# Kernel tuning notes

Hardware: AMD Instinct MI355X
Metric: run time of the kernel (lower is better)

Reference implementation:

```python
import jax, jax.numpy as jnp
import numpy as np

FEATURE_DIM, HIDDEN_DIM, ATTN_DIM = 2048, 1024, 1024
B, L = 128, 196


def setup_inputs() -> dict:
    key = jax.random.key(0)
    ks = jax.random.split(key, 8)
    s_enc = 1.0 / np.sqrt(FEATURE_DIM)
    s_hid = 1.0 / np.sqrt(HIDDEN_DIM)
    s_full = 1.0 / np.sqrt(ATTN_DIM)
    return {
        "encoder_out": jax.random.normal(ks[0], (B, L, FEATURE_DIM), jnp.float32),
        "hidden": jax.random.normal(ks[1], (B, HIDDEN_DIM), jnp.float32),
        "W_enc": jax.random.uniform(ks[2], (FEATURE_DIM, ATTN_DIM), jnp.float32, -s_enc, s_enc),
        "b_enc": jax.random.uniform(ks[3], (ATTN_DIM,), jnp.float32, -s_enc, s_enc),
        "W_hid": jax.random.uniform(ks[4], (HIDDEN_DIM, ATTN_DIM), jnp.float32, -s_hid, s_hid),
        "b_hid": jax.random.uniform(ks[5], (ATTN_DIM,), jnp.float32, -s_hid, s_hid),
        "W_full": jax.random.uniform(ks[6], (ATTN_DIM,), jnp.float32, -s_full, s_full),
        "b_full": jax.random.uniform(ks[7], (1,), jnp.float32, -s_full, s_full),
    }


def reference(encoder_out, hidden, W_enc, b_enc, W_hid, b_hid, W_full, b_full):
    # attn1: (B, L, A)
    attn1 = jnp.einsum("blf,fa->bla", encoder_out, W_enc) + b_enc
    # attn2: (B, 1, A)
    attn2 = (hidden @ W_hid + b_hid)[:, None, :]
    attn = jax.nn.relu(attn1 + attn2)
    # scalar score per location: (B, L)
    scores = jnp.einsum("bla,a->bl", attn, W_full) + b_full[0]
    alpha = jax.nn.softmax(scores, axis=1)
    # weighted sum over L: (B, F)
    context = jnp.einsum("blf,bl->bf", encoder_out, alpha)
    return context, alpha
```

## Files before the change

kernel.cpp:

```cpp
#include <hip/hip_runtime.h>
#include <hip/hip_bf16.h>

typedef unsigned short u16;
typedef short s16x8 __attribute__((ext_vector_type(8)));
typedef unsigned int u32x2 __attribute__((ext_vector_type(2)));
typedef unsigned int u32x4 __attribute__((ext_vector_type(4)));
typedef float f32x4 __attribute__((ext_vector_type(4)));

#define F_DIM 2048
#define A_DIM 1024
#define H_DIM 1024
#define BATCH 128
#define LLEN  196
#define MROWS (BATCH * LLEN)
#define MTILES (MROWS / 256)

__device__ __forceinline__ u16 f2b(float x) {
  union { float f; unsigned int u; } c; c.f = x;
  unsigned int r = (c.u + 0x7fffu + ((c.u >> 16) & 1u)) >> 16;
  return (u16)r;
}

__device__ __forceinline__ unsigned int f2b_pk(float a, float b) {
  unsigned int r;
  asm volatile("v_cvt_pk_bf16_f32 %0, %1, %2" : "=v"(r) : "v"(a), "v"(b));
  return r;
}

__device__ __forceinline__ void gload_lds16(const void* g, void* l) {
  __builtin_amdgcn_global_load_lds((const __attribute__((address_space(1))) void*)g,
                                   (__attribute__((address_space(3))) void*)l, 16, 0, 0);
}

__global__ __launch_bounds__(256) void prep_kernel(
    const float* __restrict__ W, u16* __restrict__ WT,
    const float* __restrict__ hidden, const float* __restrict__ W_hid,
    const float* __restrict__ b_hid, const float* __restrict__ b_enc,
    float* __restrict__ attn2p,
    const float* __restrict__ enc, u16* __restrict__ encB) {
  int t = threadIdx.x;
  if (blockIdx.x < 2048) {
    __shared__ float tile[32][33];
    int id = blockIdx.x;
    int kb = (id & 63) * 32, ab = (id >> 6) * 32;
    int r = t >> 3, c = (t & 7) * 4;
    float4 v = *(const float4*)&W[(size_t)(kb + r) * A_DIM + ab + c];
    tile[r][c] = v.x; tile[r][c + 1] = v.y; tile[r][c + 2] = v.z; tile[r][c + 3] = v.w;
    __syncthreads();
    ushort4 o;
    o.x = f2b(tile[c + 0][r]);
    o.y = f2b(tile[c + 1][r]);
    o.z = f2b(tile[c + 2][r]);
    o.w = f2b(tile[c + 3][r]);
    *(ushort4*)&WT[(size_t)(ab + r) * F_DIM + kb + c] = o;
  } else if (blockIdx.x < 2560) {
    __shared__ float hl[8][128];
    int id = blockIdx.x - 2048;
    int a  = (id & 3) * 256 + t;
    int b0 = ((id >> 2) & 15) * 8;
    int k0 = (id >> 6) * 128;
    {
      int j = t >> 5, kk = (t & 31) * 4;
      float4 v = *(const float4*)&hidden[(size_t)(b0 + j) * H_DIM + k0 + kk];
      hl[j][kk + 0] = v.x; hl[j][kk + 1] = v.y; hl[j][kk + 2] = v.z; hl[j][kk + 3] = v.w;
    }
    __syncthreads();
    float acc[8] = {0.f, 0.f, 0.f, 0.f, 0.f, 0.f, 0.f, 0.f};
    #pragma unroll 4
    for (int k = 0; k < 128; ++k) {
      float w = W_hid[(size_t)(k0 + k) * A_DIM + a];
      #pragma unroll
      for (int j = 0; j < 8; ++j) acc[j] = fmaf(hl[j][k], w, acc[j]);
    }
    if ((id >> 6) == 0) {
      float bias = b_hid[a] + b_enc[a];
      #pragma unroll
      for (int j = 0; j < 8; ++j) acc[j] += bias;
    }
    #pragma unroll
    for (int j = 0; j < 8; ++j) atomicAdd(&attn2p[(size_t)(b0 + j) * A_DIM + a], acc[j]);
  } else {
    const size_t n8 = (size_t)MROWS * F_DIM / 8;
    size_t gid = (size_t)(blockIdx.x - 2560) * 256 + t;
    for (size_t k = gid; k < n8; k += (size_t)2048 * 256) {
      const float4* sp = (const float4*)enc + k * 2;
      float4 a = sp[0], b = sp[1];
      u32x4 w;
      w.x = f2b_pk(a.x, a.y); w.y = f2b_pk(a.z, a.w);
      w.z = f2b_pk(b.x, b.y); w.w = f2b_pk(b.z, b.w);
      *(u32x4*)(encB + k * 8) = w;
    }
  }
}

__global__ __launch_bounds__(512, 2) void gemm_score_a(
    const u16* __restrict__ encB, const u16* __restrict__ WT,
    const float* __restrict__ attn2p, const float* __restrict__ W_full,
    float* __restrict__ scores) {
  __shared__ __align__(16) u16 As[4 * 8192];
  __shared__ __align__(16) u16 Bs[4 * 8192];

  int i = blockIdx.x;
  int g = i >> 5, r = i & 31;
  int y = r >> 3, gi = r & 7;
  int mt = g * 8 + gi;
  if (mt >= MTILES) return;
  int m0 = mt * 256, n0 = y * 256;
  int t = threadIdx.x;
  int lane = t & 63, wave = t >> 6;
  int wr = wave >> 2, wc = wave & 3;
  int c16 = lane & 15, quad = lane >> 4;

  const u16* agp = encB + (size_t)(m0 + (t >> 2)) * F_DIM + ((t & 3) ^ ((t >> 3) & 3)) * 8;
  const u16* bgp = WT   + (size_t)(n0 + (t >> 2)) * F_DIM + ((t & 3) ^ ((t >> 3) & 3)) * 8;

  const int gsw = (quad ^ ((c16 >> 1) & 3)) * 8;
  const int aro = (wr * 128 + c16) * 32;
  const int bro = (wc * 64 + c16) * 32;

  f32x4 acc[8][4];
  #pragma unroll
  for (int mi = 0; mi < 8; ++mi)
    #pragma unroll
    for (int ni = 0; ni < 4; ++ni) acc[mi][ni] = (f32x4){0.f, 0.f, 0.f, 0.f};

  s16x8 af[4], bf[4];

#define AGL(cb, kt_) do {                                                       \
    _Pragma("unroll")                                                           \
    for (int s_ = 0; s_ < 2; ++s_)                                              \
      gload_lds16(agp + (size_t)s_ * 128 * F_DIM + (size_t)(kt_) * 32,          \
                  As + (cb) * 8192 + s_ * 4096 + wave * 512);                   \
  } while (0)

#define BGL(cb, kt_) do {                                                       \
    _Pragma("unroll")                                                           \
    for (int s_ = 0; s_ < 2; ++s_)                                              \
      gload_lds16(bgp + (size_t)s_ * 128 * F_DIM + (size_t)(kt_) * 32,          \
                  Bs + (cb) * 8192 + s_ * 4096 + wave * 512);                   \
  } while (0)

#define DSRA(cb, mh)                                                            \
    _Pragma("unroll")                                                           \
    for (int i_ = 0; i_ < 4; ++i_)                                              \
      af[i_] = *(const s16x8*)&As[(cb) * 8192 + aro + ((mh) * 4 + i_) * 512 + gsw];

#define DSRB(cb)                                                                \
    _Pragma("unroll")                                                           \
    for (int j_ = 0; j_ < 4; ++j_)                                              \
      bf[j_] = *(const s16x8*)&Bs[(cb) * 8192 + bro + j_ * 512 + gsw];

#define PHTAIL(mh) do {                                                         \
    __builtin_amdgcn_s_barrier();                                               \
    asm volatile("s_waitcnt lgkmcnt(0)" ::: "memory");                          \
    __builtin_amdgcn_s_setprio(1);                                              \
    _Pragma("unroll")                                                           \
    for (int i_ = 0; i_ < 4; ++i_)                                              \
      _Pragma("unroll")                                                         \
      for (int j_ = 0; j_ < 4; ++j_)                                            \
        acc[(mh) * 4 + i_][j_] =                                                \
            __builtin_amdgcn_mfma_f32_16x16x32_bf16(                            \
                af[i_], bf[j_], acc[(mh) * 4 + i_][j_], 0, 0, 0);               \
    __builtin_amdgcn_s_setprio(0);                                              \
    __builtin_amdgcn_s_barrier();                                               \
  } while (0)

#define TILE(T_, RB_, WB_) do {                                                 \
    int kS_ = min((T_) + 2, 63);                                                \
     DSRA(RB_, 0); DSRB(RB_); AGL(WB_, kS_); PHTAIL(0);                 \
     DSRA(RB_, 1); BGL(WB_, kS_);                                       \
    asm volatile("s_waitcnt vmcnt(4)" ::: "memory");                            \
    PHTAIL(1);                                                                  \
  } while (0)

  AGL(0, 0); BGL(0, 0);
  AGL(1, 1); BGL(1, 1);
  asm volatile("s_waitcnt vmcnt(4)" ::: "memory");
  __builtin_amdgcn_s_barrier();

  #pragma unroll 1
  for (int T = 0; T < 64; T += 4) {
    TILE(T,     0, 2);
    TILE(T + 1, 1, 3);
    TILE(T + 2, 2, 0);
    TILE(T + 3, 3, 1);
  }
#undef TILE
#undef PHTAIL
#undef DSRA
#undef DSRB
#undef BGL
#undef AGL

  int bfirst = m0 / LLEN;
  int bnd1 = (bfirst + 1) * LLEN, bnd2 = (bfirst + 2) * LLEN;
  int b1c = min(bfirst + 1, BATCH - 1), b2c = min(bfirst + 2, BATCH - 1);
  float wf[4], a2v0[4], a2v1[4], a2v2[4];
  #pragma unroll
  for (int ni = 0; ni < 4; ++ni) {
    int col = n0 + wc * 64 + ni * 16 + c16;
    wf[ni]   = W_full[col];
    a2v0[ni] = attn2p[(size_t)bfirst * A_DIM + col];
    a2v1[ni] = attn2p[(size_t)b1c * A_DIM + col];
    a2v2[ni] = attn2p[(size_t)b2c * A_DIM + col];
  }
  #pragma unroll
  for (int mi = 0; mi < 8; ++mi) {
    #pragma unroll
    for (int rr = 0; rr < 4; ++rr) {
      int row_g = m0 + wr * 128 + mi * 16 + quad * 4 + rr;
      float p = 0.f;
      #pragma unroll
      for (int ni = 0; ni < 4; ++ni) {
        float a2 = row_g >= bnd1 ? (row_g >= bnd2 ? a2v2[ni] : a2v1[ni]) : a2v0[ni];
        float v = acc[mi][ni][rr] + a2;
        v = fmaxf(v, 0.f);
        p = fmaf(v, wf[ni], p);
      }
      p += __shfl_xor(p, 1);
      p += __shfl_xor(p, 2);
      p += __shfl_xor(p, 4);
      p += __shfl_xor(p, 8);
      if (c16 == 0) atomicAdd(&scores[row_g], p);
    }
  }
}

__global__ __launch_bounds__(512, 2) void gemm_score_b(
    const float* __restrict__ enc, const u16* __restrict__ WT,
    const float* __restrict__ attn2p, const float* __restrict__ W_full,
    float* __restrict__ scores) {
  __shared__ __align__(16) u16 As[2 * 16384];
  __shared__ __align__(16) u16 Bs[2 * 16384];

  int i = blockIdx.x;
  int g = i >> 5, r = i & 31;
  int y = r >> 3, gi = r & 7;
  int mt = g * 8 + gi;
  if (mt >= MTILES) return;
  int m0 = mt * 256, n0 = y * 256;
  int t = threadIdx.x;
  int lane = t & 63, wave = t >> 6;
  int wr = wave >> 2, wc = wave & 3;
  int c16 = lane & 15, quad = lane >> 4;

  const float* aP = enc + (size_t)(m0 + (t >> 2)) * F_DIM + (t & 3) * 4;
  int awo[4];
  #pragma unroll
  for (int s = 0; s < 4; ++s)
    awo[s] = (t >> 2) * 64 + ((t & 3) & 1) * 4
           + (((s * 2 + ((t & 3) >> 1)) ^ ((t >> 2) & 7)) * 8);
  const u16* bgp = WT + (size_t)(n0 + (t >> 3)) * F_DIM + ((t & 7) ^ ((t >> 3) & 7)) * 8;

  const int akey = c16 & 7;
  int gsw[2];
  gsw[0] = ((0 * 4 + quad) ^ akey) * 8;
  gsw[1] = ((1 * 4 + quad) ^ akey) * 8;
  const int aro = (wr * 128 + c16) * 64;
  const int bro = (wc * 64 + c16) * 64;

  f32x4 acc[8][4];
  #pragma unroll
  for (int mi = 0; mi < 8; ++mi)
    #pragma unroll
    for (int ni = 0; ni < 4; ++ni) acc[mi][ni] = (f32x4){0.f, 0.f, 0.f, 0.f};

  s16x8 af[4][2], bf[2][2];
  float4 R0lo[4], R0hi[4], R1lo[4], R1hi[4];

#define ALD(RX, half, kt_) do {                                                 \
    const float* p_ = aP + (size_t)(half) * 128 * F_DIM + (kt_) * 64;           \
    RX[0] = *(const float4*)(p_);                                               \
    RX[1] = *(const float4*)(p_ + 16);                                          \
    RX[2] = *(const float4*)(p_ + 32);                                          \
    RX[3] = *(const float4*)(p_ + 48);                                          \
  } while (0)

#define AWR(RX, cb, half) do {                                                  \
    _Pragma("unroll")                                                           \
    for (int s_ = 0; s_ < 4; ++s_) {                                            \
      u32x2 w_; w_.x = f2b_pk(RX[s_].x, RX[s_].y);                              \
      w_.y = f2b_pk(RX[s_].z, RX[s_].w);                                        \
      *(u32x2*)&As[(cb) * 16384 + (half) * 8192 + awo[s_]] = w_;                \
    }                                                                           \
  } while (0)

#define BGL(cb, kt_) do {                                                       \
    _Pragma("unroll")                                                           \
    for (int s_ = 0; s_ < 4; ++s_)                                              \
      gload_lds16(bgp + (size_t)s_ * 64 * F_DIM + (size_t)(kt_) * 64,           \
                  Bs + (cb) * 16384 + s_ * 4096 + wave * 512);                  \
  } while (0)

#define DSRA(cb, mh)                                                            \
    _Pragma("unroll")                                                           \
    for (int i_ = 0; i_ < 4; ++i_)                                              \
      _Pragma("unroll")                                                         \
      for (int h_ = 0; h_ < 2; ++h_)                                            \
        af[i_][h_] = *(const s16x8*)&As[(cb) * 16384 + aro                      \
                                        + ((mh) * 4 + i_) * 1024 + gsw[h_]];

#define DSRB(cb, nh)                                                            \
    _Pragma("unroll")                                                           \
    for (int j_ = 0; j_ < 2; ++j_)                                              \
      _Pragma("unroll")                                                         \
      for (int h_ = 0; h_ < 2; ++h_)                                            \
        bf[j_][h_] = *(const s16x8*)&Bs[(cb) * 16384 + bro                      \
                                        + ((nh) * 2 + j_) * 1024 + gsw[h_]];

#define PHTAIL(mh, nh) do {                                                     \
    __builtin_amdgcn_s_barrier();                                               \
    asm volatile("s_waitcnt lgkmcnt(0)" ::: "memory");                          \
    __builtin_amdgcn_s_setprio(1);                                              \
    _Pragma("unroll")                                                           \
    for (int i_ = 0; i_ < 4; ++i_)                                              \
      _Pragma("unroll")                                                         \
      for (int j_ = 0; j_ < 2; ++j_)                                            \
        _Pragma("unroll")                                                       \
        for (int h_ = 0; h_ < 2; ++h_)                                          \
          acc[(mh) * 4 + i_][(nh) * 2 + j_] =                                   \
              __builtin_amdgcn_mfma_f32_16x16x32_bf16(                          \
                  af[i_][h_], bf[j_][h_],                                       \
                  acc[(mh) * 4 + i_][(nh) * 2 + j_], 0, 0, 0);                  \
    __builtin_amdgcn_s_setprio(0);                                              \
    __builtin_amdgcn_s_barrier();                                               \
  } while (0)

#define GROUP(T_, RB_, WB_, WLO_, WHI_, LLO_, LHI_) do {                        \
    int kB_ = min((T_) + 1, 31);                                                \
    int kA_ = min((T_) + 2, 31);                                                \
     DSRA(RB_, 0); DSRB(RB_, 0); AWR(WLO_, WB_, 0); BGL(WB_, kB_);      \
    PHTAIL(0, 0);                                                               \
     DSRB(RB_, 1); AWR(WHI_, WB_, 1); ALD(LLO_, 0, kA_);                \
    PHTAIL(0, 1);                                                               \
     DSRA(RB_, 1); DSRB(RB_, 0); ALD(LHI_, 1, kA_);                     \
    PHTAIL(1, 0);                                                               \
     DSRB(RB_, 1);                                                      \
    asm volatile("s_waitcnt vmcnt(8)" ::: "memory");                            \
    PHTAIL(1, 1);                                                               \
  } while (0)

  ALD(R0lo, 0, 0);
  ALD(R0hi, 1, 0);
  BGL(0, 0);
  asm volatile("s_waitcnt vmcnt(4)" ::: "memory");
  AWR(R0lo, 0, 0);
  AWR(R0hi, 0, 1);
  ALD(R1lo, 0, 1);
  ALD(R1hi, 1, 1);
  asm volatile("s_waitcnt vmcnt(8) lgkmcnt(0)" ::: "memory");
  __builtin_amdgcn_s_barrier();

  #pragma unroll 1
  for (int T = 0; T < 32; T += 2) {
    GROUP(T,     0, 1, R1lo, R1hi, R0lo, R0hi);
    GROUP(T + 1, 1, 0, R0lo, R0hi, R1lo, R1hi);
  }
#undef GROUP
#undef PHTAIL
#undef DSRA
#undef DSRB
#undef BGL
#undef AWR
#undef ALD

  int bfirst = m0 / LLEN;
  int bnd1 = (bfirst + 1) * LLEN, bnd2 = (bfirst + 2) * LLEN;
  int b1c = min(bfirst + 1, BATCH - 1), b2c = min(bfirst + 2, BATCH - 1);
  float wf[4], a2v0[4], a2v1[4], a2v2[4];
  #pragma unroll
  for (int ni = 0; ni < 4; ++ni) {
    int col = n0 + wc * 64 + ni * 16 + c16;
    wf[ni]   = W_full[col];
    a2v0[ni] = attn2p[(size_t)bfirst * A_DIM + col];
    a2v1[ni] = attn2p[(size_t)b1c * A_DIM + col];
    a2v2[ni] = attn2p[(size_t)b2c * A_DIM + col];
  }
  #pragma unroll
  for (int mi = 0; mi < 8; ++mi) {
    #pragma unroll
    for (int rr = 0; rr < 4; ++rr) {
      int row_g = m0 + wr * 128 + mi * 16 + quad * 4 + rr;
      float p = 0.f;
      #pragma unroll
      for (int ni = 0; ni < 4; ++ni) {
        float a2 = row_g >= bnd1 ? (row_g >= bnd2 ? a2v2[ni] : a2v1[ni]) : a2v0[ni];
        float v = acc[mi][ni][rr] + a2;
        v = fmaxf(v, 0.f);
        p = fmaf(v, wf[ni], p);
      }
      p += __shfl_xor(p, 1);
      p += __shfl_xor(p, 2);
      p += __shfl_xor(p, 4);
      p += __shfl_xor(p, 8);
      if (c16 == 0) atomicAdd(&scores[row_g], p);
    }
  }
}

__global__ __launch_bounds__(256) void context_kernel(
    const float* __restrict__ enc, const float* __restrict__ scores,
    float* __restrict__ alpha_out, float* __restrict__ out) {
  __shared__ float al[LLEN];
  __shared__ float red[8];
  __shared__ float4 part[4][64];
  int b = blockIdx.y, t = threadIdx.x;
  float s = (t < LLEN) ? scores[b * LLEN + t] : -3.0e38f;
  float m = s;
  #pragma unroll
  for (int o = 1; o <= 32; o <<= 1) m = fmaxf(m, __shfl_xor(m, o));
  if ((t & 63) == 0) red[t >> 6] = m;
  __syncthreads();
  m = fmaxf(fmaxf(red[0], red[1]), fmaxf(red[2], red[3]));
  float e = (t < LLEN) ? expf(s - m) : 0.f;
  float sum = e;
  #pragma unroll
  for (int o = 1; o <= 32; o <<= 1) sum += __shfl_xor(sum, o);
  if ((t & 63) == 0) red[4 + (t >> 6)] = sum;
  __syncthreads();
  sum = red[4] + red[5] + red[6] + red[7];
  float av = e / sum;
  if (t < LLEN) {
    al[t] = av;
    if (blockIdx.x == 0) alpha_out[b * LLEN + t] = av;
  }
  __syncthreads();
  int f4 = blockIdx.x * 64 + (t & 63);
  int lq = t >> 6;
  const float4* e4 = (const float4*)enc
                   + ((size_t)b * LLEN + lq * 49) * (F_DIM / 4) + f4;
  float4 acc = {0.f, 0.f, 0.f, 0.f};
  #pragma unroll 7
  for (int j = 0; j < 49; ++j) {
    float4 v = e4[(size_t)j * (F_DIM / 4)];
    float a = al[lq * 49 + j];
    acc.x = fmaf(v.x, a, acc.x);
    acc.y = fmaf(v.y, a, acc.y);
    acc.z = fmaf(v.z, a, acc.z);
    acc.w = fmaf(v.w, a, acc.w);
  }
  part[lq][t & 63] = acc;
  __syncthreads();
  if (t < 64) {
    float4 p0 = part[0][t], p1 = part[1][t], p2 = part[2][t], p3 = part[3][t];
    float4 sv;
    sv.x = (p0.x + p1.x) + (p2.x + p3.x);
    sv.y = (p0.y + p1.y) + (p2.y + p3.y);
    sv.z = (p0.z + p1.z) + (p2.z + p3.z);
    sv.w = (p0.w + p1.w) + (p2.w + p3.w);
    *(float4*)(out + (size_t)b * F_DIM + (size_t)(blockIdx.x * 64 + t) * 4) = sv;
  }
}

extern "C" void kernel_launch(void* const* d_in, const int* in_sizes, int n_in,
                              void* d_out, int out_size, void* d_ws, size_t ws_size,
                              hipStream_t stream) {
  const float* enc    = (const float*)d_in[0];
  const float* hidden = (const float*)d_in[1];
  const float* W_enc  = (const float*)d_in[2];
  const float* b_enc  = (const float*)d_in[3];
  const float* W_hid  = (const float*)d_in[4];
  const float* b_hid  = (const float*)d_in[5];
  const float* W_full = (const float*)d_in[6];
  float* out = (float*)d_out;
  float* alpha_out = out + (size_t)BATCH * F_DIM;

  const size_t wt_bytes   = (size_t)A_DIM * F_DIM * sizeof(u16);
  const size_t a2_bytes   = (size_t)BATCH * A_DIM * sizeof(float);
  const size_t sc_bytes   = (size_t)MROWS * sizeof(float);
  const size_t encb_bytes = (size_t)MROWS * F_DIM * sizeof(u16);
  char* ws = (char*)d_ws;
  u16*   WT     = (u16*)ws;
  float* attn2p = (float*)(ws + wt_bytes);
  float* scores = (float*)(ws + wt_bytes + a2_bytes);
  u16*   encB   = (u16*)(ws + wt_bytes + a2_bytes + sc_bytes);

  const bool bigws = ws_size >= wt_bytes + a2_bytes + sc_bytes + encb_bytes;

  hipMemsetAsync(attn2p, 0, a2_bytes + sc_bytes, stream);

  if (bigws) {
    prep_kernel<<<dim3(2048 + 512 + 2048), 256, 0, stream>>>(
        W_enc, WT, hidden, W_hid, b_hid, b_enc, attn2p, enc, encB);
    gemm_score_a<<<dim3(416), 512, 0, stream>>>(encB, WT, attn2p, W_full, scores);
  } else {
    prep_kernel<<<dim3(2048 + 512), 256, 0, stream>>>(
        W_enc, WT, hidden, W_hid, b_hid, b_enc, attn2p, enc, encB);
    gemm_score_b<<<dim3(416), 512, 0, stream>>>(enc, WT, attn2p, W_full, scores);
  }
  context_kernel<<<dim3(8, BATCH), 256, 0, stream>>>(enc, scores, alpha_out, out);
}
```

Before: 476.6 us.

## Double-buffer LDS fragment registers to overlap ds_reads with MFMA in GEMM loop

Restructures the bf16 GEMM main loop so A and B fragments for the next half-tile or next k-tile are read from LDS into a second register set while the current MFMAs run. Partial lgkmcnt/vmcnt waits replace full drains, and a prologue preloads the first fragments. This aims to hide LDS read latency behind matrix work, at the cost of more VGPRs and more delicate barrier and waitcnt ordering that could introduce races or reduce occupancy.

```diff
diff --git a/kernel.cpp b/kernel.cpp
--- a/kernel.cpp
+++ b/kernel.cpp
@@ -124,7 +124,7 @@
     #pragma unroll
     for (int ni = 0; ni < 4; ++ni) acc[mi][ni] = (f32x4){0.f, 0.f, 0.f, 0.f};
 
-  s16x8 af[4], bf[4];
+  s16x8 afA[4], afB[4], bfA[4], bfB[4];
 
 #define AGL(cb, kt_) do {                                                       \
     _Pragma("unroll")                                                           \
@@ -140,19 +140,17 @@
                   Bs + (cb) * 8192 + s_ * 4096 + wave * 512);                   \
   } while (0)
 
-#define DSRA(cb, mh)                                                            \
+#define DSRA(DST, cb, mh)                                                       \
     _Pragma("unroll")                                                           \
     for (int i_ = 0; i_ < 4; ++i_)                                              \
-      af[i_] = *(const s16x8*)&As[(cb) * 8192 + aro + ((mh) * 4 + i_) * 512 + gsw];
-
-#define DSRB(cb)                                                                \
+      DST[i_] = *(const s16x8*)&As[(cb) * 8192 + aro + ((mh) * 4 + i_) * 512 + gsw];
+
+#define DSRB(DST, cb)                                                           \
     _Pragma("unroll")                                                           \
     for (int j_ = 0; j_ < 4; ++j_)                                              \
-      bf[j_] = *(const s16x8*)&Bs[(cb) * 8192 + bro + j_ * 512 + gsw];
-
-#define PHTAIL(mh) do {                                                         \
-    __builtin_amdgcn_s_barrier();                                               \
-    asm volatile("s_waitcnt lgkmcnt(0)" ::: "memory");                          \
+      DST[j_] = *(const s16x8*)&Bs[(cb) * 8192 + bro + j_ * 512 + gsw];
+
+#define MFMA16(AF, BF, mh) do {                                                 \
     __builtin_amdgcn_s_setprio(1);                                              \
     _Pragma("unroll")                                                           \
     for (int i_ = 0; i_ < 4; ++i_)                                              \
@@ -160,33 +158,44 @@
       for (int j_ = 0; j_ < 4; ++j_)                                            \
         acc[(mh) * 4 + i_][j_] =                                                \
             __builtin_amdgcn_mfma_f32_16x16x32_bf16(                            \
-                af[i_], bf[j_], acc[(mh) * 4 + i_][j_], 0, 0, 0);               \
+                AF[i_], BF[j_], acc[(mh) * 4 + i_][j_], 0, 0, 0);               \
     __builtin_amdgcn_s_setprio(0);                                              \
+  } while (0)
+
+#define TILE(T_, RB_, WB_, NB_, BFC_, BFN_) do {                                \
+    int kS_ = min((T_) + 2, 63);                                                \
+                                                                        \
+    DSRA(afB, RB_, 1);                                                          \
+    AGL(WB_, kS_);                                                              \
+    asm volatile("s_waitcnt vmcnt(2)" ::: "memory");                            \
     __builtin_amdgcn_s_barrier();                                               \
-  } while (0)
-
-#define TILE(T_, RB_, WB_) do {                                                 \
-    int kS_ = min((T_) + 2, 63);                                                \
-     DSRA(RB_, 0); DSRB(RB_); AGL(WB_, kS_); PHTAIL(0);                 \
-     DSRA(RB_, 1); BGL(WB_, kS_);                                       \
-    asm volatile("s_waitcnt vmcnt(4)" ::: "memory");                            \
-    PHTAIL(1);                                                                  \
+    asm volatile("s_waitcnt lgkmcnt(4)" ::: "memory");                          \
+    MFMA16(afA, BFC_, 0);                                                       \
+                                                                        \
+    DSRA(afA, NB_, 0);                                                          \
+    DSRB(BFN_, NB_);                                                            \
+    BGL(WB_, kS_);                                                              \
+    __builtin_amdgcn_s_barrier();                                               \
+    asm volatile("s_waitcnt lgkmcnt(8)" ::: "memory");                          \
+    MFMA16(afB, BFC_, 1);                                                       \
   } while (0)
 
   AGL(0, 0); BGL(0, 0);
   AGL(1, 1); BGL(1, 1);
   asm volatile("s_waitcnt vmcnt(4)" ::: "memory");
   __builtin_amdgcn_s_barrier();
+  DSRA(afA, 0, 0);
+  DSRB(bfA, 0);
 
   #pragma unroll 1
   for (int T = 0; T < 64; T += 4) {
-    TILE(T,     0, 2);
-    TILE(T + 1, 1, 3);
-    TILE(T + 2, 2, 0);
-    TILE(T + 3, 3, 1);
+    TILE(T,     0, 2, 1, bfA, bfB);
+    TILE(T + 1, 1, 3, 2, bfB, bfA);
+    TILE(T + 2, 2, 0, 3, bfA, bfB);
+    TILE(T + 3, 3, 1, 0, bfB, bfA);
   }
 #undef TILE
-#undef PHTAIL
+#undef MFMA16
 #undef DSRA
 #undef DSRB
 #undef BGL
@@ -249,7 +258,7 @@
   #pragma unroll
   for (int s = 0; s < 4; ++s)
     awo[s] = (t >> 2) * 64 + ((t & 3) & 1) * 4
-           + (((s * 2 + ((t & 3) >> 1)) ^ ((t >> 2) & 7)) * 8);
+           + (((s * 2 + ((t & 3) >> 1)) ^ (((t >> 2) >> 0) & 7)) * 8);
   const u16* bgp = WT + (size_t)(n0 + (t >> 3)) * F_DIM + ((t & 7) ^ ((t >> 3) & 7)) * 8;
 
   const int akey = c16 & 7;
```

Result: no change. 480.5 us (+0.8%).
